# Optimization experiments

Measured on AMD Instinct MI355X. Metric: run time of the kernel, lower is better.

The kernel has to match this reference:

```python
import jax, jax.numpy as jnp
import numpy as np

N, T, D, H = 256, 128, 512, 1024


def setup_inputs() -> dict:
    key = jax.random.key(0)
    k_x, k_A, k_Wx, k_Wh, k_Wa = jax.random.split(key, 5)
    x = jax.random.normal(k_x, (N, T, D), dtype=jnp.float32)
    A = jax.random.normal(k_A, (N, H, 4, 4), dtype=jnp.float32)
    Wx = jax.random.normal(k_Wx, (D, 4 * H), dtype=jnp.float32) / np.sqrt(D)
    Wh = jax.random.normal(k_Wh, (H, 4 * H), dtype=jnp.float32) / np.sqrt(H)
    Wattn = jax.random.normal(k_Wa, (H, 4 * H), dtype=jnp.float32) / np.sqrt(H)
    b = jnp.zeros((4 * H,), dtype=jnp.float32)
    return {"x": x, "A": A, "Wx": Wx, "Wh": Wh, "Wattn": Wattn, "b": b}


def _attention_lstm(x, A, Wx, Wh, Wattn, b):
    # A: (N, H, 4, 4) -> flatten spatial to (N, H, 16)
    A_flat = A.reshape(A.shape[0], A.shape[1], -1)
    h0 = A_flat.mean(axis=2)  # (N, H)
    c0 = h0
    Hdim = h0.shape[1]
    scale = 1.0 / jnp.sqrt(jnp.asarray(Hdim, dtype=x.dtype))

    def step(carry, x_t):
        prev_h, prev_c = carry
        # scaled dot-product attention over 16 spatial locations
        scores = jnp.einsum("nh,nhs->ns", prev_h, A_flat) * scale  # (N, 16)
        w = jax.nn.softmax(scores, axis=1)
        attn = jnp.einsum("nhs,ns->nh", A_flat, w)  # (N, H)
        # fused LSTM gates
        a = x_t @ Wx + prev_h @ Wh + attn @ Wattn + b  # (N, 4H)
        i = jax.nn.sigmoid(a[:, 0:Hdim])
        f = jax.nn.sigmoid(a[:, Hdim:2 * Hdim])
        o = jax.nn.sigmoid(a[:, 2 * Hdim:3 * Hdim])
        g = jnp.tanh(a[:, 3 * Hdim:4 * Hdim])
        next_c = f * prev_c + i * g
        next_h = o * jnp.tanh(next_c)
        return (next_h, next_c), next_h

    x_tnd = jnp.swapaxes(x, 0, 1)  # (T, N, D)
    _, h_tnh = jax.lax.scan(step, (h0, c0), x_tnd)
    return jnp.swapaxes(h_tnh, 0, 1)  # (N, T, H)


def reference(x, A, Wx, Wh, Wattn, b):
    return _attention_lstm(x, A, Wx, Wh, Wattn, b)
```

## Files before the change

kernel.cpp:

```cpp
#include <hip/hip_runtime.h>
#include <math.h>

#define NB 256
#define TT 128
#define DD 512
#define HH 1024
#define KHX 1536
#define KFB 2560
#define BK 128
#define NBLK6 256
#define SCSLOT 32768
#define HSLOT (NB * HH)

typedef _Float16 half_t;
typedef _Float16 half8 __attribute__((ext_vector_type(8)));
typedef _Float16 half4v __attribute__((ext_vector_type(4)));
typedef _Float16 half2v __attribute__((ext_vector_type(2)));
typedef float f32x4 __attribute__((ext_vector_type(4)));


__global__ __launch_bounds__(256) void k_trans(const float* __restrict__ src,
        half_t* __restrict__ dst, int kstride, int koff, int nkt) {
    __shared__ half_t tile[64][65];
    int bk = blockIdx.x % nkt;
    int bn = blockIdx.x / nkt;
    int k0 = bk * 64, n0 = bn * 64;
    #pragma unroll
    for (int i = 0; i < 16; ++i) {
        int idx = i * 256 + threadIdx.x;
        int r = idx >> 6, c = idx & 63;
        tile[c][r] = (half_t)src[(size_t)(k0 + r) * 4096 + n0 + c];
    }
    __syncthreads();
    #pragma unroll
    for (int i = 0; i < 16; ++i) {
        int idx = i * 256 + threadIdx.x;
        int r = idx >> 6, c = idx & 63;
        dst[(size_t)(n0 + r) * kstride + koff + k0 + c] = tile[r][c];
    }
}

__global__ __launch_bounds__(256) void k_convX(const float* __restrict__ x,
        half_t* __restrict__ x16) {
    size_t base = ((size_t)blockIdx.x * 256 + threadIdx.x) * 32;
    #pragma unroll
    for (int u = 0; u < 4; ++u) {
        float4 a = ((const float4*)(x + base))[2 * u];
        float4 c = ((const float4*)(x + base))[2 * u + 1];
        half8 p;
        p[0] = (half_t)a.x; p[1] = (half_t)a.y; p[2] = (half_t)a.z; p[3] = (half_t)a.w;
        p[4] = (half_t)c.x; p[5] = (half_t)c.y; p[6] = (half_t)c.z; p[7] = (half_t)c.w;
        ((half8*)(x16 + base))[u] = p;
    }
}

__global__ __launch_bounds__(256) void k_convA2(const float* __restrict__ A,
        half_t* __restrict__ A16, half_t* __restrict__ AsT,
        float* __restrict__ cbuf, half_t* __restrict__ h16) {
    int n = blockIdx.x, tid = threadIdx.x;
    #pragma unroll
    for (int r = 0; r < 4; ++r) {
        int h = tid + r * 256;
        const float4* ap = (const float4*)(A + ((size_t)n * HH + h) * 16);
        float4 v0 = ap[0], v1 = ap[1], v2 = ap[2], v3 = ap[3];
        float a[16];
        a[0]=v0.x; a[1]=v0.y; a[2] =v0.z; a[3] =v0.w;
        a[4]=v1.x; a[5]=v1.y; a[6] =v1.z; a[7] =v1.w;
        a[8]=v2.x; a[9]=v2.y; a[10]=v2.z; a[11]=v2.w;
        a[12]=v3.x; a[13]=v3.y; a[14]=v3.z; a[15]=v3.w;
        float hv = 0.f;
        #pragma unroll
        for (int s = 0; s < 16; ++s) hv += a[s];
        hv *= (1.f / 16.f);
        size_t ci = (size_t)n * HH + h;
        cbuf[ci] = hv;
        h16[ci] = (half_t)hv;
        half8 q0, q1;
        #pragma unroll
        for (int s = 0; s < 8; ++s) { q0[s] = (half_t)a[s]; q1[s] = (half_t)a[s + 8]; }
        *(half8*)(A16 + ci * 16) = q0;
        *(half8*)(A16 + ci * 16 + 8) = q1;
        #pragma unroll
        for (int s = 0; s < 16; ++s)
            AsT[(size_t)n * 16 * HH + (size_t)s * HH + h] = (half_t)a[s];
    }
}

__global__ __launch_bounds__(256) void k_initsc(const half_t* __restrict__ h16,
        const half_t* __restrict__ A16,
        float* __restrict__ sc0, float* __restrict__ sc1, float* __restrict__ sc2) {
    __shared__ float sred[4][16];
    int n = blockIdx.x, tid = threadIdx.x;
    float ps[16];
    #pragma unroll
    for (int s = 0; s < 16; ++s) ps[s] = 0.f;
    #pragma unroll
    for (int r = 0; r < 4; ++r) {
        int h = tid + r * 256;
        size_t ci = (size_t)n * HH + h;
        float hv = (float)h16[ci];
        const half8* ap = (const half8*)(A16 + ci * 16);
        half8 a0 = ap[0], a1 = ap[1];
        #pragma unroll
        for (int s = 0; s < 8; ++s) {
            ps[s]     += hv * (float)a0[s];
            ps[s + 8] += hv * (float)a1[s];
        }
    }
    #pragma unroll
    for (int off = 32; off; off >>= 1)
        #pragma unroll
        for (int s = 0; s < 16; ++s) ps[s] += __shfl_xor(ps[s], off, 64);
    int wave = tid >> 6;
    if ((tid & 63) == 0)
        #pragma unroll
        for (int s = 0; s < 16; ++s) sred[wave][s] = ps[s];
    __syncthreads();
    if (tid < 16)
        sc0[(size_t)n * 16 + tid] =
            sred[0][tid] + sred[1][tid] + sred[2][tid] + sred[3][tid];
    if (tid < 112) {
        int x = 1 + tid / 16, s = tid % 16;
        sc0[((size_t)x * 256 + n) * 16 + s] = 0.f;
    }
    if (tid < 128) {
        int x = tid / 16, s = tid % 16;
        sc1[((size_t)x * 256 + n) * 16 + s] = 0.f;
        sc2[((size_t)x * 256 + n) * 16 + s] = 0.f;
    }
}

__global__ __launch_bounds__(256) void k_gemm_G(const half_t* __restrict__ AsT,
        const half_t* __restrict__ WaT, half_t* __restrict__ G16) {
    __shared__ half_t sAs[16][BK + 8];
    __shared__ half_t sB[4][16][BK + 8];
    int bid = blockIdx.x;
    int n = bid >> 6, jt = bid & 63;
    int j0 = jt * 16;
    int tid = threadIdx.x, wv = tid >> 6, lane = tid & 63;
    f32x4 acc = {};
    int srB = tid >> 2, scB = (tid & 3) * 32;
    int gB = srB >> 4, jcB = srB & 15;
    for (int it = 0; it < HH / BK; ++it) {
        int k0 = it * BK;
        if (tid < 128) {
            int r = tid >> 3, c = (tid & 7) * 16;
            const uint4* sp = (const uint4*)(AsT + (size_t)n * 16 * HH + (size_t)r * HH + k0 + c);
            uint4 u0 = sp[0], u1 = sp[1];
            *(uint4*)&sAs[r][c] = u0;
            *(uint4*)&sAs[r][c + 8] = u1;
        }
        {
            const half_t* src = WaT + ((size_t)(gB * HH + j0 + jcB)) * HH + k0 + scB;
            uint4 u0 = ((const uint4*)src)[0];
            uint4 u1 = ((const uint4*)src)[1];
            uint4 u2 = ((const uint4*)src)[2];
            uint4 u3 = ((const uint4*)src)[3];
            *((uint4*)&sB[gB][jcB][scB])      = u0;
            *((uint4*)&sB[gB][jcB][scB + 8])  = u1;
            *((uint4*)&sB[gB][jcB][scB + 16]) = u2;
            *((uint4*)&sB[gB][jcB][scB + 24]) = u3;
        }
        __syncthreads();
        int row16 = lane & 15, kg = lane >> 4;
        #pragma unroll
        for (int kc = 0; kc < BK / 32; ++kc) {
            half8 bf = *(const half8*)&sB[wv][row16][kc * 32 + kg * 8];
            half8 af = *(const half8*)&sAs[row16][kc * 32 + kg * 8];
            acc = __builtin_amdgcn_mfma_f32_16x16x32_f16(af, bf, acc, 0, 0, 0);
        }
        __syncthreads();
    }
    int col = lane & 15, rbase = (lane >> 4) * 4;
    size_t jf = (size_t)wv * HH + j0 + col;
    half4v o;
    o[0] = (half_t)acc[0]; o[1] = (half_t)acc[1];
    o[2] = (half_t)acc[2]; o[3] = (half_t)acc[3];
    *(half4v*)(G16 + ((size_t)n * 4096 + jf) * 16 + rbase) = o;
}

__global__ __launch_bounds__(256) void k_gemm_XW2(const half_t* __restrict__ x16,
        const half_t* __restrict__ WhxT, half_t* __restrict__ XW16) {
    __shared__ half_t sA[128][520];
    __shared__ half_t sB[128][72];
    int bm = blockIdx.x;
    int row0 = bm * 128;
    int tid = threadIdx.x, wv = tid >> 6, lane = tid & 63;
    int la = lane & 15, kg = lane >> 4;
    int mh = wv & 1, jh = wv >> 1;
    {
        int r = tid >> 1, hseg = tid & 1;
        const uint4* src = (const uint4*)(x16 + (size_t)(row0 + r) * DD + hseg * 256);
        #pragma unroll
        for (int i = 0; i < 16; ++i)
            *(uint4*)&sA[r][hseg * 256 + i * 8] = src[i];
    }
    __syncthreads();
    int srB = tid >> 2, scB = (tid & 3) * 16;
    for (int bj = 0; bj < 64; ++bj) {
        f32x4 acc[4][2] = {};
        for (int c = 0; c < 8; ++c) {
            {
                const uint4* sp = (const uint4*)(WhxT + (size_t)(bj * 64 + srB) * KHX + c * 64 + scB);
                *(uint4*)&sB[srB][scB] = sp[0];
            }
            __syncthreads();
            #pragma unroll
            for (int ks = 0; ks < 2; ++ks) {
                half8 b0 = *(const half8*)&sB[jh * 32 + la][ks * 32 + kg * 8];
                half8 b1 = *(const half8*)&sB[jh * 32 + 16 + la][ks * 32 + kg * 8];
                #pragma unroll
                for (int m = 0; m < 4; ++m) {
                    half8 af = *(const half8*)&sA[mh * 64 + m * 16 + la][c * 64 + ks * 32 + kg * 8];
                    acc[m][0] = __builtin_amdgcn_mfma_f32_16x16x32_f16(af, b0, acc[m][0], 0, 0, 0);
                    acc[m][1] = __builtin_amdgcn_mfma_f32_16x16x32_f16(af, b1, acc[m][1], 0, 0, 0);
                }
            }
            __syncthreads();
        }
        #pragma unroll
        for (int m = 0; m < 4; ++m)
            #pragma unroll
            for (int jt = 0; jt < 2; ++jt)
                #pragma unroll
                for (int q = 0; q < 4; ++q) {
                    int rl = mh * 64 + m * 16 + kg * 4 + q;
                    int cl = jh * 32 + jt * 16 + la;
                    sB[rl][cl] = (half_t)acc[m][jt][q];
                }
        __syncthreads();
        int col0 = bj * 64;
        int g = col0 >> 10;
        #pragma unroll
        for (int i = 0; i < 4; ++i) {
            int idx = tid + i * 256;
            int rl = idx >> 3, grp = idx & 7;
            int R = row0 + rl;
            int t = R & 127, nn = R >> 7;
            int mh2 = nn >> 7, nl2 = nn & 127;
            int jb2 = ((col0 & 1023) >> 3) + grp;
            size_t dst = ((((size_t)t * 128 + jb2) * 2 + mh2) * 128 + nl2) * 32 + g * 8;
            *(half8*)(XW16 + dst) = *(const half8*)&sB[rl][grp * 8];
        }
        __syncthreads();
    }
}


__global__ __launch_bounds__(512, 1) void k_steps6(
        const half_t* __restrict__ XW16, half_t* __restrict__ hh,
        const half_t* __restrict__ WhxT, const half_t* __restrict__ A16,
        const half_t* __restrict__ G16, const float* __restrict__ b,
        const float* __restrict__ cbuf, float* __restrict__ scr,
        float* __restrict__ out, int* __restrict__ bar) {
    __shared__ half_t W[32][1028];
    __shared__ float sm[4][128][16];
    __shared__ float pe[128][33];
    __shared__ float ps[2][128][18];

    int bid = blockIdx.x;
    int mhalf = bid & 1, jb = bid >> 1;
    int n0 = mhalf * 128;
    int tid = threadIdx.x;
    int wv = tid >> 6, lane = tid & 63;
    int la = lane & 15, kg = lane >> 4;
    int slice = bid & 7;
    int* hcnt = bar + mhalf * 32;

    {
        int wr = tid >> 4, seg = tid & 15;
        const half_t* wsrc = WhxT + (size_t)((wr >> 3) * HH + jb * 8 + (wr & 7)) * KHX
                           + DD + seg * 64;
        #pragma unroll
        for (int i = 0; i < 8; ++i)
            *(uint4*)&W[wr][seg * 64 + i * 8] = ((const uint4*)wsrc)[i];
    }

    int n_l = tid & 127, jg2 = tid >> 7;
    int n = n0 + n_l;
    int jbase = jb * 8 + jg2 * 2;
    half8 gq[4][4];
    #pragma unroll
    for (int g = 0; g < 4; ++g) {
        const half8* gsrc = (const half8*)(G16 + ((size_t)n * 4096 + g * HH + jbase) * 16);
        #pragma unroll
        for (int i = 0; i < 4; ++i) gq[g][i] = gsrc[i];
    }
    half8 aq[4];
    {
        const half8* asrc = (const half8*)(A16 + ((size_t)n * HH + jbase) * 16);
        #pragma unroll
        for (int i = 0; i < 4; ++i) aq[i] = asrc[i];
    }
    float bb[4][2];
    #pragma unroll
    for (int g = 0; g < 4; ++g) {
        bb[g][0] = b[g * HH + jbase];
        bb[g][1] = b[g * HH + jbase + 1];
    }
    float creg[2];
    creg[0] = cbuf[(size_t)n * HH + jbase];
    creg[1] = cbuf[(size_t)n * HH + jbase + 1];

    __threadfence();
    __syncthreads();

    for (int t = 0; t < TT; ++t) {
        const half_t* hcur = hh + (size_t)t * HSLOT;
        unsigned* hnext = (unsigned*)(hh + (size_t)(t + 1) * HSLOT);
        const float* scc = scr + (size_t)t * SCSLOT;
        float* scn = scr + (size_t)(t + 1) * SCSLOT;

        half2v xwv[4];
        {
            const half_t* xwp = XW16 + ((((size_t)t * 128 + jb) * 2 + mhalf) * 128 + n_l) * 32;
            #pragma unroll
            for (int g = 0; g < 4; ++g) xwv[g] = *(const half2v*)(xwp + g * 8 + jg2 * 2);
        }

        if (t > 0) {
            int tgt = 4 * t;
            int guard = 0;
            for (;;) {
                int v = (lane < 32)
                    ? __hip_atomic_load(&hcnt[lane], __ATOMIC_RELAXED, __HIP_MEMORY_SCOPE_AGENT)
                    : tgt;
                if (__all(v >= tgt)) break;
                __builtin_amdgcn_s_sleep(2);
                if (++guard > (1 << 18)) break;
            }
        }
        __builtin_amdgcn_sched_barrier(0);

        {
            const float* p0 = scc + ((size_t)(jg2 * 2) * 256 + n) * 16;
            const float* p1 = scc + ((size_t)(jg2 * 2 + 1) * 256 + n) * 16;
            #pragma unroll
            for (int i = 0; i < 4; ++i) {
                float4 a = ((const float4*)p0)[i];
                float4 c = ((const float4*)p1)[i];
                float4 o;
                o.x = a.x + c.x; o.y = a.y + c.y; o.z = a.z + c.z; o.w = a.w + c.w;
                *(float4*)&sm[jg2][n_l][4 * i] = o;
            }
        }
        __syncthreads();
        float w16[16];
        {
            float sc[16];
            #pragma unroll
            for (int i = 0; i < 4; ++i) {
                float4 q0 = *(const float4*)&sm[0][n_l][4 * i];
                float4 q1 = *(const float4*)&sm[1][n_l][4 * i];
                float4 q2 = *(const float4*)&sm[2][n_l][4 * i];
                float4 q3 = *(const float4*)&sm[3][n_l][4 * i];
                sc[4 * i + 0] = q0.x + q1.x + q2.x + q3.x;
                sc[4 * i + 1] = q0.y + q1.y + q2.y + q3.y;
                sc[4 * i + 2] = q0.z + q1.z + q2.z + q3.z;
                sc[4 * i + 3] = q0.w + q1.w + q2.w + q3.w;
            }
            float m = -1e30f;
            #pragma unroll
            for (int s = 0; s < 16; ++s) { sc[s] *= 0.03125f; m = fmaxf(m, sc[s]); }
            float den = 0.f;
            #pragma unroll
            for (int s = 0; s < 16; ++s) { sc[s] = expf(sc[s] - m); den += sc[s]; }
            float inv = 1.f / den;
            #pragma unroll
            for (int s = 0; s < 16; ++s) w16[s] = sc[s] * inv;
        }

        f32x4 acc0 = {}, acc1 = {};
        {
            const half_t* hrow = hcur + (size_t)(n0 + wv * 16 + la) * HH + kg * 8;
            #pragma unroll
            for (int c = 0; c < 32; ++c) {
                half8 af = *(const half8*)(hrow + c * 32);
                half8 b0 = *(const half8*)&W[la][c * 32 + kg * 8];
                half8 b1 = *(const half8*)&W[16 + la][c * 32 + kg * 8];
                acc0 = __builtin_amdgcn_mfma_f32_16x16x32_f16(af, b0, acc0, 0, 0, 0);
                acc1 = __builtin_amdgcn_mfma_f32_16x16x32_f16(af, b1, acc1, 0, 0, 0);
            }
        }

        __syncthreads();
        #pragma unroll
        for (int q = 0; q < 4; ++q) {
            pe[wv * 16 + kg * 4 + q][la]      = acc0[q];
            pe[wv * 16 + kg * 4 + q][16 + la] = acc1[q];
        }
        __syncthreads();

        float v[4][2];
        #pragma unroll
        for (int g = 0; g < 4; ++g) {
            #pragma unroll
            for (int jj = 0; jj < 2; ++jj) {
                float a0 = 0.f;
                #pragma unroll
                for (int s = 0; s < 16; ++s)
                    a0 += w16[s] * (float)gq[g][jj * 2 + (s >> 3)][s & 7];
                v[g][jj] = pe[n_l][g * 8 + jg2 * 2 + jj] + bb[g][jj]
                         + (float)xwv[g][jj] + a0;
            }
        }
        float hv[2];
        #pragma unroll
        for (int jj = 0; jj < 2; ++jj) {
            float ig = 1.f / (1.f + expf(-v[0][jj]));
            float fg = 1.f / (1.f + expf(-v[1][jj]));
            float og = 1.f / (1.f + expf(-v[2][jj]));
            float gg = tanhf(v[3][jj]);
            float cn = fg * creg[jj] + ig * gg;
            creg[jj] = cn;
            hv[jj] = og * tanhf(cn);
        }
        {
            float2 o2; o2.x = hv[0]; o2.y = hv[1];
            *(float2*)(out + ((size_t)n * TT + t) * HH + jbase) = o2;
            union { half2v h2; unsigned u; } cv;
            cv.h2[0] = (half_t)hv[0]; cv.h2[1] = (half_t)hv[1];
            __hip_atomic_store(hnext + (((size_t)n * HH + jbase) >> 1), cv.u,
                               __ATOMIC_RELAXED, __HIP_MEMORY_SCOPE_AGENT);
        }
        float p[16];
        #pragma unroll
        for (int s = 0; s < 16; ++s)
            p[s] = hv[0] * (float)aq[s >> 3][s & 7]
                 + hv[1] * (float)aq[2 + (s >> 3)][s & 7];
        int pair = jg2 >> 1;
        if ((jg2 & 1) == 0) {
            #pragma unroll
            for (int s = 0; s < 16; ++s) ps[pair][n_l][s] = p[s];
        }
        __syncthreads();
        if ((jg2 & 1) == 1) {
            #pragma unroll
            for (int s = 0; s < 16; ++s) ps[pair][n_l][s] += p[s];
        }
        __syncthreads();
        #pragma unroll
        for (int i = 0; i < 4; ++i) {
            int slot = tid * 4 + i;
            int nn = slot >> 4, s = slot & 15;
            atomicAdd(scn + ((size_t)slice * 256 + n0 + nn) * 16 + s,
                      ps[0][nn][s] + ps[1][nn][s]);
        }

        __syncthreads();
        if (tid == 0)
            __hip_atomic_fetch_add(&hcnt[jb >> 2], 1, __ATOMIC_RELAXED,
                                   __HIP_MEMORY_SCOPE_AGENT);
    }
}


__global__ __launch_bounds__(256) void k_convA(const float* __restrict__ A,
        half_t* __restrict__ A16, half_t* __restrict__ AsT,
        float* __restrict__ cbuf, half_t* __restrict__ h16,
        float* __restrict__ sc0, float* __restrict__ sc1, float* __restrict__ sc2) {
    __shared__ float sred[4][16];
    int n = blockIdx.x, tid = threadIdx.x;
    float ps[16];
    #pragma unroll
    for (int s = 0; s < 16; ++s) ps[s] = 0.f;
    #pragma unroll
    for (int r = 0; r < 4; ++r) {
        int h = tid + r * 256;
        const float4* ap = (const float4*)(A + ((size_t)n * HH + h) * 16);
        float4 v0 = ap[0], v1 = ap[1], v2 = ap[2], v3 = ap[3];
        float a[16];
        a[0]=v0.x; a[1]=v0.y; a[2] =v0.z; a[3] =v0.w;
        a[4]=v1.x; a[5]=v1.y; a[6] =v1.z; a[7] =v1.w;
        a[8]=v2.x; a[9]=v2.y; a[10]=v2.z; a[11]=v2.w;
        a[12]=v3.x; a[13]=v3.y; a[14]=v3.z; a[15]=v3.w;
        float hv = 0.f;
        #pragma unroll
        for (int s = 0; s < 16; ++s) hv += a[s];
        hv *= (1.f / 16.f);
        size_t ci = (size_t)n * HH + h;
        cbuf[ci] = hv;
        h16[ci] = (half_t)hv;
        half8 q0, q1;
        #pragma unroll
        for (int s = 0; s < 8; ++s) { q0[s] = (half_t)a[s]; q1[s] = (half_t)a[s + 8]; }
        *(half8*)(A16 + ci * 16) = q0;
        *(half8*)(A16 + ci * 16 + 8) = q1;
        #pragma unroll
        for (int s = 0; s < 16; ++s)
            AsT[(size_t)n * 16 * HH + (size_t)s * HH + h] = (half_t)a[s];
        #pragma unroll
        for (int s = 0; s < 16; ++s) ps[s] += hv * a[s];
    }
    #pragma unroll
    for (int off = 32; off; off >>= 1)
        #pragma unroll
        for (int s = 0; s < 16; ++s) ps[s] += __shfl_xor(ps[s], off, 64);
    int wave = tid >> 6;
    if ((tid & 63) == 0)
        #pragma unroll
        for (int s = 0; s < 16; ++s) sred[wave][s] = ps[s];
    __syncthreads();
    if (tid < 16) {
        sc0[n * 16 + tid] = sred[0][tid] + sred[1][tid] + sred[2][tid] + sred[3][tid];
        sc1[n * 16 + tid] = 0.f;
        sc2[n * 16 + tid] = 0.f;
    }
}

union LdsS {
    struct {
        half_t sA[32][BK + 8];
        half_t sB[4][16][BK + 8];
    } s;
    float pe[4][32][16];
};

__global__ __launch_bounds__(256) void k_step(const float* __restrict__ x,
        const half_t* __restrict__ h16c, half_t* __restrict__ h16n,
        const half_t* __restrict__ WhxT, const half_t* __restrict__ A16,
        const half_t* __restrict__ G16, const float* __restrict__ b,
        float* __restrict__ cbuf, const float* __restrict__ scC,
        float* __restrict__ scN, float* __restrict__ scZ,
        float* __restrict__ out, int t) {
    __shared__ LdsS L;
    __shared__ float wlds[32][16];
    int bid = blockIdx.x;
    int xcd = bid & 7, slot = bid >> 3;
    int mtile = slot & 7, jtile = slot >> 3;
    int n0 = mtile * 32;
    int j0 = xcd * 128 + jtile * 16;
    int tid = threadIdx.x, wv = tid >> 6, lane = tid & 63;

    if (bid < 16) scZ[bid * 256 + tid] = 0.f;
    if (tid < 32) {
        int n = n0 + tid;
        const float4* sp = (const float4*)(scC + n * 16);
        float4 u0 = sp[0], u1 = sp[1], u2 = sp[2], u3 = sp[3];
        float sc[16] = {u0.x, u0.y, u0.z, u0.w, u1.x, u1.y, u1.z, u1.w,
                        u2.x, u2.y, u2.z, u2.w, u3.x, u3.y, u3.z, u3.w};
        float m = -1e30f;
        #pragma unroll
        for (int s = 0; s < 16; ++s) { sc[s] *= 0.03125f; m = fmaxf(m, sc[s]); }
        float den = 0.f;
        #pragma unroll
        for (int s = 0; s < 16; ++s) { sc[s] = expf(sc[s] - m); den += sc[s]; }
        float inv = 1.f / den;
        #pragma unroll
        for (int s = 0; s < 16; ++s) wlds[tid][s] = sc[s] * inv;
    }

    f32x4 acc[2] = {};
    int srA = tid >> 3, scA = (tid & 7) * 16;
    int srB = tid >> 2, scB = (tid & 3) * 32;
    int gB = srB >> 4, jcB = srB & 15;

    for (int it = 0; it < KHX / BK; ++it) {
        int k0 = it * BK;
        {
            int n = n0 + srA;
            if (k0 < DD) {
                const float* src = x + ((size_t)n * TT + t) * DD + k0 + scA;
                float4 v0 = ((const float4*)src)[0];
                float4 v1 = ((const float4*)src)[1];
                float4 v2 = ((const float4*)src)[2];
                float4 v3 = ((const float4*)src)[3];
                half8 p0, p1;
                p0[0] = (half_t)v0.x; p0[1] = (half_t)v0.y; p0[2] = (half_t)v0.z; p0[3] = (half_t)v0.w;
                p0[4] = (half_t)v1.x; p0[5] = (half_t)v1.y; p0[6] = (half_t)v1.z; p0[7] = (half_t)v1.w;
                p1[0] = (half_t)v2.x; p1[1] = (half_t)v2.y; p1[2] = (half_t)v2.z; p1[3] = (half_t)v2.w;
                p1[4] = (half_t)v3.x; p1[5] = (half_t)v3.y; p1[6] = (half_t)v3.z; p1[7] = (half_t)v3.w;
                *(half8*)&L.s.sA[srA][scA]     = p0;
                *(half8*)&L.s.sA[srA][scA + 8] = p1;
            } else {
                const half_t* srch = h16c + (size_t)n * HH + (k0 - DD) + scA;
                uint4 u0 = ((const uint4*)srch)[0];
                uint4 u1 = ((const uint4*)srch)[1];
                *((uint4*)&L.s.sA[srA][scA])     = u0;
                *((uint4*)&L.s.sA[srA][scA + 8]) = u1;
            }
        }
        {
            const half_t* src = WhxT + ((size_t)(gB * HH + j0 + jcB)) * KHX + k0 + scB;
            uint4 u0 = ((const uint4*)src)[0];
            uint4 u1 = ((const uint4*)src)[1];
            uint4 u2 = ((const uint4*)src)[2];
            uint4 u3 = ((const uint4*)src)[3];
            *((uint4*)&L.s.sB[gB][jcB][scB])      = u0;
            *((uint4*)&L.s.sB[gB][jcB][scB + 8])  = u1;
            *((uint4*)&L.s.sB[gB][jcB][scB + 16]) = u2;
            *((uint4*)&L.s.sB[gB][jcB][scB + 24]) = u3;
        }
        __syncthreads();
        int row16 = lane & 15, kg = lane >> 4;
        #pragma unroll
        for (int kc = 0; kc < BK / 32; ++kc) {
            half8 bf = *(const half8*)&L.s.sB[wv][row16][kc * 32 + kg * 8];
            #pragma unroll
            for (int m = 0; m < 2; ++m) {
                half8 af = *(const half8*)&L.s.sA[row16 + m * 16][kc * 32 + kg * 8];
                acc[m] = __builtin_amdgcn_mfma_f32_16x16x32_f16(af, bf, acc[m], 0, 0, 0);
            }
        }
        __syncthreads();
    }
    {
        int col = lane & 15, rbase = (lane >> 4) * 4;
        #pragma unroll
        for (int m = 0; m < 2; ++m)
            #pragma unroll
            for (int q = 0; q < 4; ++q)
                L.pe[wv][m * 16 + rbase + q][col] = acc[m][q];
    }
    __syncthreads();
    #pragma unroll
    for (int q2 = 0; q2 < 2; ++q2) {
        int idx = tid + q2 * 256;
        int r = idx >> 4, jc = idx & 15;
        int n = n0 + r, j = j0 + jc;
        float wv16[16];
        #pragma unroll
        for (int s = 0; s < 16; ++s) wv16[s] = wlds[r][s];
        float v[4];
        v[0] = L.pe[0][r][jc] + b[j];
        v[1] = L.pe[1][r][jc] + b[HH + j];
        v[2] = L.pe[2][r][jc] + b[2 * HH + j];
        v[3] = L.pe[3][r][jc] + b[3 * HH + j];
        #pragma unroll
        for (int g = 0; g < 4; ++g) {
            const half8* gq = (const half8*)(G16 + ((size_t)n * 4096 + g * HH + j) * 16);
            half8 ga = gq[0], gb2 = gq[1];
            float a0 = 0.f;
            #pragma unroll
            for (int s = 0; s < 8; ++s)
                a0 += wv16[s] * (float)ga[s] + wv16[s + 8] * (float)gb2[s];
            v[g] += a0;
        }
        float ig = 1.f / (1.f + expf(-v[0]));
        float fg = 1.f / (1.f + expf(-v[1]));
        float og = 1.f / (1.f + expf(-v[2]));
        float gg = tanhf(v[3]);
        size_t ci = (size_t)n * HH + j;
        float cp = cbuf[ci];
        float cn = fg * cp + ig * gg;
        cbuf[ci] = cn;
        float hv = og * tanhf(cn);
        out[((size_t)n * TT + t) * HH + j] = hv;
        h16n[ci] = (half_t)hv;
        const half8* ap = (const half8*)(A16 + ci * 16);
        half8 a0 = ap[0], a1 = ap[1];
        float p[16];
        #pragma unroll
        for (int s = 0; s < 8; ++s) { p[s] = hv * (float)a0[s]; p[s + 8] = hv * (float)a1[s]; }
        #pragma unroll
        for (int msk = 1; msk < 16; msk <<= 1)
            #pragma unroll
            for (int s = 0; s < 16; ++s) p[s] += __shfl_xor(p[s], msk, 64);
        float myp = 0.f;
        #pragma unroll
        for (int s = 0; s < 16; ++s) myp = (jc == s) ? p[s] : myp;
        atomicAdd(scN + n * 16 + jc, myp);
    }
}


__global__ __launch_bounds__(256) void fb_wconv(const float* __restrict__ Wx,
        const float* __restrict__ Wh, const float* __restrict__ Wa,
        half_t* __restrict__ WT) {
    __shared__ half_t tile[64][65];
    int bk = blockIdx.x % 40;
    int bn = blockIdx.x / 40;
    int k0 = bk * 64, n0 = bn * 64;
    #pragma unroll
    for (int i = 0; i < 16; ++i) {
        int idx = i * 256 + threadIdx.x;
        int r = idx >> 6, c = idx & 63;
        int k = k0 + r, n = n0 + c;
        float v;
        if (k < DD)            v = Wx[(size_t)k * 4096 + n];
        else if (k < DD + HH)  v = Wh[(size_t)(k - DD) * 4096 + n];
        else                   v = Wa[(size_t)(k - DD - HH) * 4096 + n];
        tile[c][r] = (half_t)v;
    }
    __syncthreads();
    #pragma unroll
    for (int i = 0; i < 16; ++i) {
        int idx = i * 256 + threadIdx.x;
        int r = idx >> 6, c = idx & 63;
        WT[(size_t)(n0 + r) * KFB + k0 + c] = tile[r][c];
    }
}

__global__ __launch_bounds__(256) void fb_init(const float* __restrict__ A,
        float* __restrict__ h0, float* __restrict__ c0) {
    int n = blockIdx.x;
    #pragma unroll
    for (int r = 0; r < 4; ++r) {
        int h = threadIdx.x + r * 256;
        const float4* ap = (const float4*)(A + ((size_t)n * HH + h) * 16);
        float s = 0.f;
        #pragma unroll
        for (int q = 0; q < 4; ++q) {
            float4 v = ap[q];
            s += v.x + v.y + v.z + v.w;
        }
        s *= (1.f / 16.f);
        h0[n * HH + h] = s;
        c0[n * HH + h] = s;
    }
}

__global__ __launch_bounds__(256) void fb_attn(const float* __restrict__ A,
        const float* __restrict__ hprev, long long hstride,
        half_t* __restrict__ h16, half_t* __restrict__ attn16) {
    __shared__ float sh[HH];
    __shared__ float sred[4][16];
    int n = blockIdx.x;
    const float* hp = hprev + (size_t)n * hstride;
    #pragma unroll
    for (int r = 0; r < 4; ++r) {
        int h = threadIdx.x + r * 256;
        float v = hp[h];
        sh[h] = v;
        h16[n * HH + h] = (half_t)v;
    }
    __syncthreads();
    float a[4][16];
    float ps[16];
    #pragma unroll
    for (int s = 0; s < 16; ++s) ps[s] = 0.f;
    #pragma unroll
    for (int r = 0; r < 4; ++r) {
        int h = threadIdx.x + r * 256;
        const float4* ap = (const float4*)(A + ((size_t)n * HH + h) * 16);
        float4 v0 = ap[0], v1 = ap[1], v2 = ap[2], v3 = ap[3];
        a[r][0] = v0.x;  a[r][1] = v0.y;  a[r][2]  = v0.z;  a[r][3]  = v0.w;
        a[r][4] = v1.x;  a[r][5] = v1.y;  a[r][6]  = v1.z;  a[r][7]  = v1.w;
        a[r][8] = v2.x;  a[r][9] = v2.y;  a[r][10] = v2.z;  a[r][11] = v2.w;
        a[r][12] = v3.x; a[r][13] = v3.y; a[r][14] = v3.z;  a[r][15] = v3.w;
        float hh = sh[h];
        #pragma unroll
        for (int s = 0; s < 16; ++s) ps[s] += hh * a[r][s];
    }
    #pragma unroll
    for (int off = 32; off; off >>= 1)
        #pragma unroll
        for (int s = 0; s < 16; ++s) ps[s] += __shfl_xor(ps[s], off, 64);
    int wave = threadIdx.x >> 6;
    if ((threadIdx.x & 63) == 0)
        #pragma unroll
        for (int s = 0; s < 16; ++s) sred[wave][s] = ps[s];
    __syncthreads();
    float sc[16], m = -1e30f;
    #pragma unroll
    for (int s = 0; s < 16; ++s) {
        sc[s] = (sred[0][s] + sred[1][s] + sred[2][s] + sred[3][s]) * 0.03125f;
        m = fmaxf(m, sc[s]);
    }
    float den = 0.f;
    #pragma unroll
    for (int s = 0; s < 16; ++s) { sc[s] = expf(sc[s] - m); den += sc[s]; }
    float inv = 1.f / den;
    #pragma unroll
    for (int r = 0; r < 4; ++r) {
        int h = threadIdx.x + r * 256;
        float acc = 0.f;
        #pragma unroll
        for (int s = 0; s < 16; ++s) acc += a[r][s] * sc[s];
        attn16[n * HH + h] = (half_t)(acc * inv);
    }
}

union LdsFB {
    struct {
        half_t sA[32][BK + 8];
        half_t sB[4][16][BK + 8];
    } s;
    float pe[4][32][16];
};

__global__ __launch_bounds__(256) void fb_gemm(const float* __restrict__ x,
        const half_t* __restrict__ h16, const half_t* __restrict__ attn16,
        const half_t* __restrict__ WT, const float* __restrict__ b,
        float* __restrict__ cbuf, float* __restrict__ out, int t) {
    __shared__ LdsFB L;
    int bid = blockIdx.x;
    int xcd = bid & 7;
    int slot = bid >> 3;
    int mtile = slot & 7;
    int jtile = slot >> 3;
    int m0 = mtile * 32;
    int j0 = xcd * 128 + jtile * 16;
    int tid = threadIdx.x;
    int wv = tid >> 6, lane = tid & 63;
    f32x4 acc[2] = {};
    int srA = tid >> 3, scA = (tid & 7) * 16;
    int srB = tid >> 2, scB = (tid & 3) * 32;
    int gB = srB >> 4, jcB = srB & 15;
    for (int it = 0; it < KFB / BK; ++it) {
        int k0 = it * BK;
        {
            int n = m0 + srA;
            if (k0 < DD) {
                const float* src = x + ((size_t)n * TT + t) * DD + k0 + scA;
                float4 v0 = ((const float4*)src)[0];
                float4 v1 = ((const float4*)src)[1];
                float4 v2 = ((const float4*)src)[2];
                float4 v3 = ((const float4*)src)[3];
                half8 p0, p1;
                p0[0] = (half_t)v0.x; p0[1] = (half_t)v0.y; p0[2] = (half_t)v0.z; p0[3] = (half_t)v0.w;
                p0[4] = (half_t)v1.x; p0[5] = (half_t)v1.y; p0[6] = (half_t)v1.z; p0[7] = (half_t)v1.w;
                p1[0] = (half_t)v2.x; p1[1] = (half_t)v2.y; p1[2] = (half_t)v2.z; p1[3] = (half_t)v2.w;
                p1[4] = (half_t)v3.x; p1[5] = (half_t)v3.y; p1[6] = (half_t)v3.z; p1[7] = (half_t)v3.w;
                *(half8*)&L.s.sA[srA][scA]     = p0;
                *(half8*)&L.s.sA[srA][scA + 8] = p1;
            } else {
                const half_t* srch = (k0 < DD + HH)
                    ? (h16    + (size_t)n * HH + (k0 - DD)      + scA)
                    : (attn16 + (size_t)n * HH + (k0 - DD - HH) + scA);
                uint4 u0 = ((const uint4*)srch)[0];
                uint4 u1 = ((const uint4*)srch)[1];
                *((uint4*)&L.s.sA[srA][scA])     = u0;
                *((uint4*)&L.s.sA[srA][scA + 8]) = u1;
            }
        }
        {
            const half_t* src = WT + ((size_t)(gB * HH + j0 + jcB)) * KFB + k0 + scB;
            uint4 u0 = ((const uint4*)src)[0];
            uint4 u1 = ((const uint4*)src)[1];
            uint4 u2 = ((const uint4*)src)[2];
            uint4 u3 = ((const uint4*)src)[3];
            *((uint4*)&L.s.sB[gB][jcB][scB])      = u0;
            *((uint4*)&L.s.sB[gB][jcB][scB + 8])  = u1;
            *((uint4*)&L.s.sB[gB][jcB][scB + 16]) = u2;
            *((uint4*)&L.s.sB[gB][jcB][scB + 24]) = u3;
        }
        __syncthreads();
        int row16 = lane & 15, kg = lane >> 4;
        #pragma unroll
        for (int kc = 0; kc < BK / 32; ++kc) {
            half8 bf = *(const half8*)&L.s.sB[wv][row16][kc * 32 + kg * 8];
            #pragma unroll
            for (int m = 0; m < 2; ++m) {
                half8 af = *(const half8*)&L.s.sA[row16 + m * 16][kc * 32 + kg * 8];
                acc[m] = __builtin_amdgcn_mfma_f32_16x16x32_f16(af, bf, acc[m], 0, 0, 0);
            }
        }
        __syncthreads();
    }
    {
        int col = lane & 15, rbase = (lane >> 4) * 4;
        #pragma unroll
        for (int m = 0; m < 2; ++m)
            #pragma unroll
            for (int q = 0; q < 4; ++q)
                L.pe[wv][m * 16 + rbase + q][col] = acc[m][q];
    }
    __syncthreads();
    #pragma unroll
    for (int q2 = 0; q2 < 2; ++q2) {
        int idx = tid + q2 * 256;
        int r = idx >> 4, jc = idx & 15;
        int n = m0 + r, j = j0 + jc;
        float vi = L.pe[0][r][jc] + b[j];
        float vf = L.pe[1][r][jc] + b[HH + j];
        float vo = L.pe[2][r][jc] + b[2 * HH + j];
        float vg = L.pe[3][r][jc] + b[3 * HH + j];
        float ig = 1.f / (1.f + expf(-vi));
        float fg = 1.f / (1.f + expf(-vf));
        float og = 1.f / (1.f + expf(-vo));
        float gg = tanhf(vg);
        size_t ci = (size_t)n * HH + j;
        float cp = cbuf[ci];
        float cn = fg * cp + ig * gg;
        cbuf[ci] = cn;
        out[((size_t)n * TT + t) * HH + j] = og * tanhf(cn);
    }
}


extern "C" void kernel_launch(void* const* d_in, const int* in_sizes, int n_in,
                              void* d_out, int out_size, void* d_ws, size_t ws_size,
                              hipStream_t stream) {
    const float* x  = (const float*)d_in[0];
    const float* A  = (const float*)d_in[1];
    const float* Wx = (const float*)d_in[2];
    const float* Wh = (const float*)d_in[3];
    const float* Wa = (const float*)d_in[4];
    const float* b  = (const float*)d_in[5];
    float* out = (float*)d_out;
    char* ws = (char*)d_ws;

    int maxb = 0;
    hipError_t oe = hipOccupancyMaxActiveBlocksPerMultiprocessor(&maxb, k_steps6, 512, 0);
    bool persistent_ok = (oe == hipSuccess && maxb >= 1);

    if (ws_size >= 460112128ULL && persistent_ok) {
        half_t* WhxT = (half_t*)(ws);
        half_t* WaT  = (half_t*)(ws + 12582912);
        half_t* A16  = (half_t*)(ws + 20971520);
        half_t* AsT  = (half_t*)(ws + 29360128);
        half_t* G16  = (half_t*)(ws + 37748736);
        float*  cb   = (float*) (ws + 72351744);
        half_t* x16  = (half_t*)(ws + 73449472);
        int*    bar  = (int*)   (ws + 107003904);
        half_t* XW16 = (half_t*)(ws + 107004160);
        half_t* HHr  = (half_t*)(ws + 375439616);
        float*  SCr  = (float*) (ws + 443072768);

        half_t* hh0 = HHr;

        hipLaunchKernelGGL(k_trans, dim3(8 * 64),  dim3(256), 0, stream, Wx, WhxT, KHX, 0,   8);
        hipLaunchKernelGGL(k_trans, dim3(16 * 64), dim3(256), 0, stream, Wh, WhxT, KHX, 512, 16);
        hipLaunchKernelGGL(k_trans, dim3(16 * 64), dim3(256), 0, stream, Wa, WaT,  HH,  0,   16);
        hipLaunchKernelGGL(k_convX, dim3(2048), dim3(256), 0, stream, x, x16);
        hipLaunchKernelGGL(k_convA2, dim3(256), dim3(256), 0, stream, A, A16, AsT, cb, hh0);
        hipLaunchKernelGGL(k_gemm_G, dim3(NB * 64), dim3(256), 0, stream, AsT, WaT, G16);
        hipLaunchKernelGGL(k_gemm_XW2, dim3(256), dim3(256), 0, stream, x16, WhxT, XW16);
        hipMemsetAsync(bar, 0, 256, stream);
        hipMemsetAsync(SCr, 0, 17039360, stream);
        hipLaunchKernelGGL(k_initsc, dim3(256), dim3(256), 0, stream, hh0, A16,
                           SCr, SCr + SCSLOT, SCr + 2 * SCSLOT);
        hipLaunchKernelGGL(k_steps6, dim3(NBLK6), dim3(512), 0, stream,
                           XW16, HHr, WhxT, A16, G16, b, cb, SCr, out, bar);
    } else if (ws_size >= 73449472ULL) {
        half_t* WhxT = (half_t*)(ws);
        half_t* WaT  = (half_t*)(ws + 12582912);
        half_t* A16  = (half_t*)(ws + 20971520);
        half_t* AsT  = (half_t*)(ws + 29360128);
        half_t* G16  = (half_t*)(ws + 37748736);
        half_t* h16a = (half_t*)(ws + 71303168);
        half_t* h16b = (half_t*)(ws + 71827456);
        float*  cb   = (float*) (ws + 72351744);
        float*  sc0  = (float*) (ws + 73400320);
        float*  sc1  = (float*) (ws + 73416704);
        float*  sc2  = (float*) (ws + 73433088);
        float* scb[3] = {sc0, sc1, sc2};

        hipLaunchKernelGGL(k_trans, dim3(8 * 64),  dim3(256), 0, stream, Wx, WhxT, KHX, 0,   8);
        hipLaunchKernelGGL(k_trans, dim3(16 * 64), dim3(256), 0, stream, Wh, WhxT, KHX, 512, 16);
        hipLaunchKernelGGL(k_trans, dim3(16 * 64), dim3(256), 0, stream, Wa, WaT,  HH,  0,   16);
        hipLaunchKernelGGL(k_convA, dim3(256), dim3(256), 0, stream,
                           A, A16, AsT, cb, h16a, sc0, sc1, sc2);
        hipLaunchKernelGGL(k_gemm_G, dim3(NB * 64), dim3(256), 0, stream, AsT, WaT, G16);
        for (int t = 0; t < TT; ++t) {
            float* scC = scb[t % 3];
            float* scN = scb[(t + 1) % 3];
            float* scZ = scb[(t + 2) % 3];
            half_t* h16c = (t & 1) ? h16b : h16a;
            half_t* h16n = (t & 1) ? h16a : h16b;
            hipLaunchKernelGGL(k_step, dim3(512), dim3(256), 0, stream,
                               x, h16c, h16n, WhxT, A16, G16, b, cb, scC, scN, scZ, out, t);
        }
    } else {
        half_t* WT  = (half_t*)ws;
        float*  h0  = (float*)(ws + 20971520);
        float*  cb  = (float*)(ws + 22020096);
        half_t* h16 = (half_t*)(ws + 23068672);
        half_t* a16 = (half_t*)(ws + 23592960);
        hipLaunchKernelGGL(fb_wconv, dim3(2560), dim3(256), 0, stream, Wx, Wh, Wa, WT);
        hipLaunchKernelGGL(fb_init, dim3(256), dim3(256), 0, stream, A, h0, cb);
        for (int t = 0; t < TT; ++t) {
            const float* hp = (t == 0) ? h0 : (out + (size_t)(t - 1) * HH);
            long long hstride = (t == 0) ? (long long)HH : (long long)TT * HH;
            hipLaunchKernelGGL(fb_attn, dim3(256), dim3(256), 0, stream, A, hp, hstride, h16, a16);
            hipLaunchKernelGGL(fb_gemm, dim3(512), dim3(256), 0, stream,
                               x, h16, a16, WT, b, cb, out, t);
        }
    }
}
```

Before: 4.635 ms.

## Compute attention scores per home row with counter sync instead of atomics

The persistent step kernel no longer builds next-step attention scores by atomically accumulating partial dot products from every block into sliced buffers. Instead, each block computes the full score vector for one batch row from the current hidden state and publishes it, and other blocks wait on a per-half counter before reading. This removes the init-score kernel, the large memset and the per-step atomicAdd traffic, at the cost of an extra spin-wait per step. The XW GEMM is also reverted to a 2D grid of small tiles, and nontemporal loads and stores are used for the XW input and the output.

```diff
diff --git a/kernel.cpp b/kernel.cpp
--- a/kernel.cpp
+++ b/kernel.cpp
@@ -8,9 +8,9 @@
 #define KHX 1536
 #define KFB 2560
 #define BK 128
-#define NBLK6 256
-#define SCSLOT 32768
+#define NBLK7 256
 #define HSLOT (NB * HH)
+#define SCSLOT2 (NB * 16)
 
 typedef _Float16 half_t;
 typedef _Float16 half8 __attribute__((ext_vector_type(8)));
@@ -83,50 +83,6 @@
         #pragma unroll
         for (int s = 0; s < 16; ++s)
             AsT[(size_t)n * 16 * HH + (size_t)s * HH + h] = (half_t)a[s];
-    }
-}
-
-__global__ __launch_bounds__(256) void k_initsc(const half_t* __restrict__ h16,
-        const half_t* __restrict__ A16,
-        float* __restrict__ sc0, float* __restrict__ sc1, float* __restrict__ sc2) {
-    __shared__ float sred[4][16];
-    int n = blockIdx.x, tid = threadIdx.x;
-    float ps[16];
-    #pragma unroll
-    for (int s = 0; s < 16; ++s) ps[s] = 0.f;
-    #pragma unroll
-    for (int r = 0; r < 4; ++r) {
-        int h = tid + r * 256;
-        size_t ci = (size_t)n * HH + h;
-        float hv = (float)h16[ci];
-        const half8* ap = (const half8*)(A16 + ci * 16);
-        half8 a0 = ap[0], a1 = ap[1];
-        #pragma unroll
-        for (int s = 0; s < 8; ++s) {
-            ps[s]     += hv * (float)a0[s];
-            ps[s + 8] += hv * (float)a1[s];
-        }
-    }
-    #pragma unroll
-    for (int off = 32; off; off >>= 1)
-        #pragma unroll
-        for (int s = 0; s < 16; ++s) ps[s] += __shfl_xor(ps[s], off, 64);
-    int wave = tid >> 6;
-    if ((tid & 63) == 0)
-        #pragma unroll
-        for (int s = 0; s < 16; ++s) sred[wave][s] = ps[s];
-    __syncthreads();
-    if (tid < 16)
-        sc0[(size_t)n * 16 + tid] =
-            sred[0][tid] + sred[1][tid] + sred[2][tid] + sred[3][tid];
-    if (tid < 112) {
-        int x = 1 + tid / 16, s = tid % 16;
-        sc0[((size_t)x * 256 + n) * 16 + s] = 0.f;
-    }
-    if (tid < 128) {
-        int x = tid / 16, s = tid % 16;
-        sc1[((size_t)x * 256 + n) * 16 + s] = 0.f;
-        sc2[((size_t)x * 256 + n) * 16 + s] = 0.f;
     }
 }
 
@@ -179,93 +135,92 @@
     *(half4v*)(G16 + ((size_t)n * 4096 + jf) * 16 + rbase) = o;
 }
 
-__global__ __launch_bounds__(256) void k_gemm_XW2(const half_t* __restrict__ x16,
+__global__ __launch_bounds__(256) void k_gemm_XW(const half_t* __restrict__ x16,
         const half_t* __restrict__ WhxT, half_t* __restrict__ XW16) {
-    __shared__ half_t sA[128][520];
-    __shared__ half_t sB[128][72];
-    int bm = blockIdx.x;
+    __shared__ half_t sA[128][72];
+    __shared__ half_t sB[64][72];
+    int bid = blockIdx.x;
+    int bm = bid & 255;
+    int bj = bid >> 8;
     int row0 = bm * 128;
+    int col0 = bj * 64;
     int tid = threadIdx.x, wv = tid >> 6, lane = tid & 63;
     int la = lane & 15, kg = lane >> 4;
     int mh = wv & 1, jh = wv >> 1;
-    {
-        int r = tid >> 1, hseg = tid & 1;
-        const uint4* src = (const uint4*)(x16 + (size_t)(row0 + r) * DD + hseg * 256);
-        #pragma unroll
-        for (int i = 0; i < 16; ++i)
-            *(uint4*)&sA[r][hseg * 256 + i * 8] = src[i];
+    f32x4 acc[4][2] = {};
+    int srA = tid >> 1, scA = (tid & 1) * 32;
+    int srB = tid >> 2, scB = (tid & 3) * 16;
+    for (int c = 0; c < 8; ++c) {
+        {
+            const uint4* sp = (const uint4*)(x16 + (size_t)(row0 + srA) * DD + c * 64 + scA);
+            uint4 u0 = sp[0], u1 = sp[1];
+            *(uint4*)&sA[srA][scA] = u0;
+            *(uint4*)&sA[srA][scA + 8] = u1;
+        }
+        {
+            const uint4* sp = (const uint4*)(WhxT + (size_t)(col0 + srB) * KHX + c * 64 + scB);
+            *(uint4*)&sB[srB][scB] = sp[0];
+        }
+        __syncthreads();
+        #pragma unroll
+        for (int ks = 0; ks < 2; ++ks) {
+            half8 b0 = *(const half8*)&sB[jh * 32 + la][ks * 32 + kg * 8];
+            half8 b1 = *(const half8*)&sB[jh * 32 + 16 + la][ks * 32 + kg * 8];
+            #pragma unroll
+            for (int m = 0; m < 4; ++m) {
+                half8 af = *(const half8*)&sA[mh * 64 + m * 16 + la][ks * 32 + kg * 8];
+                acc[m][0] = __builtin_amdgcn_mfma_f32_16x16x32_f16(af, b0, acc[m][0], 0, 0, 0);
+                acc[m][1] = __builtin_amdgcn_mfma_f32_16x16x32_f16(af, b1, acc[m][1], 0, 0, 0);
+            }
+        }
+        __syncthreads();
     }
     __syncthreads();
-    int srB = tid >> 2, scB = (tid & 3) * 16;
-    for (int bj = 0; bj < 64; ++bj) {
-        f32x4 acc[4][2] = {};
-        for (int c = 0; c < 8; ++c) {
-            {
-                const uint4* sp = (const uint4*)(WhxT + (size_t)(bj * 64 + srB) * KHX + c * 64 + scB);
-                *(uint4*)&sB[srB][scB] = sp[0];
-            }
-            __syncthreads();
-            #pragma unroll
-            for (int ks = 0; ks < 2; ++ks) {
-                half8 b0 = *(const half8*)&sB[jh * 32 + la][ks * 32 + kg * 8];
-                half8 b1 = *(const half8*)&sB[jh * 32 + 16 + la][ks * 32 + kg * 8];
-                #pragma unroll
-                for (int m = 0; m < 4; ++m) {
-                    half8 af = *(const half8*)&sA[mh * 64 + m * 16 + la][c * 64 + ks * 32 + kg * 8];
-                    acc[m][0] = __builtin_amdgcn_mfma_f32_16x16x32_f16(af, b0, acc[m][0], 0, 0, 0);
-                    acc[m][1] = __builtin_amdgcn_mfma_f32_16x16x32_f16(af, b1, acc[m][1], 0, 0, 0);
-                }
-            }
-            __syncthreads();
-        }
-        #pragma unroll
-        for (int m = 0; m < 4; ++m)
-            #pragma unroll
-            for (int jt = 0; jt < 2; ++jt)
-                #pragma unroll
-                for (int q = 0; q < 4; ++q) {
-                    int rl = mh * 64 + m * 16 + kg * 4 + q;
-                    int cl = jh * 32 + jt * 16 + la;
-                    sB[rl][cl] = (half_t)acc[m][jt][q];
-                }
-        __syncthreads();
-        int col0 = bj * 64;
-        int g = col0 >> 10;
-        #pragma unroll
-        for (int i = 0; i < 4; ++i) {
-            int idx = tid + i * 256;
-            int rl = idx >> 3, grp = idx & 7;
-            int R = row0 + rl;
-            int t = R & 127, nn = R >> 7;
-            int mh2 = nn >> 7, nl2 = nn & 127;
-            int jb2 = ((col0 & 1023) >> 3) + grp;
-            size_t dst = ((((size_t)t * 128 + jb2) * 2 + mh2) * 128 + nl2) * 32 + g * 8;
-            *(half8*)(XW16 + dst) = *(const half8*)&sB[rl][grp * 8];
-        }
-        __syncthreads();
-    }
-}
-
-
-__global__ __launch_bounds__(512, 1) void k_steps6(
+    half_t (*Cl)[72] = sA;
+    #pragma unroll
+    for (int m = 0; m < 4; ++m)
+        #pragma unroll
+        for (int jt = 0; jt < 2; ++jt)
+            #pragma unroll
+            for (int q = 0; q < 4; ++q) {
+                int rl = mh * 64 + m * 16 + kg * 4 + q;
+                int cl = jh * 32 + jt * 16 + la;
+                Cl[rl][cl] = (half_t)acc[m][jt][q];
+            }
+    __syncthreads();
+    int g = col0 >> 10;
+    #pragma unroll
+    for (int i = 0; i < 4; ++i) {
+        int idx = tid + i * 256;
+        int rl = idx >> 3, grp = idx & 7;
+        int R = row0 + rl;
+        int t = R & 127, nn = R >> 7;
+        int mh2 = nn >> 7, nl2 = nn & 127;
+        int jb2 = ((col0 & 1023) >> 3) + grp;
+        size_t dst = ((((size_t)t * 128 + jb2) * 2 + mh2) * 128 + nl2) * 32 + g * 8;
+        *(half8*)(XW16 + dst) = *(const half8*)&Cl[rl][grp * 8];
+    }
+}
+
+
+__global__ __launch_bounds__(512, 1) void k_steps7(
         const half_t* __restrict__ XW16, half_t* __restrict__ hh,
         const half_t* __restrict__ WhxT, const half_t* __restrict__ A16,
         const half_t* __restrict__ G16, const float* __restrict__ b,
         const float* __restrict__ cbuf, float* __restrict__ scr,
         float* __restrict__ out, int* __restrict__ bar) {
     __shared__ half_t W[32][1028];
-    __shared__ float sm[4][128][16];
+    __shared__ float red[8][16];
     __shared__ float pe[128][33];
-    __shared__ float ps[2][128][18];
 
     int bid = blockIdx.x;
     int mhalf = bid & 1, jb = bid >> 1;
     int n0 = mhalf * 128;
     int tid = threadIdx.x;
-    int wv = tid >> 6, lane = tid & 63;
+    int wvi = tid >> 6, lane = tid & 63;
     int la = lane & 15, kg = lane >> 4;
-    int slice = bid & 7;
     int* hcnt = bar + mhalf * 32;
+    int* scnt = bar + 64 + mhalf * 32;
 
     {
         int wr = tid >> 4, seg = tid & 15;
@@ -278,6 +233,7 @@
 
     int n_l = tid & 127, jg2 = tid >> 7;
     int n = n0 + n_l;
+    int n_home = n0 + jb;
     int jbase = jb * 8 + jg2 * 2;
     half8 gq[4][4];
     #pragma unroll
@@ -285,12 +241,6 @@
         const half8* gsrc = (const half8*)(G16 + ((size_t)n * 4096 + g * HH + jbase) * 16);
         #pragma unroll
         for (int i = 0; i < 4; ++i) gq[g][i] = gsrc[i];
-    }
-    half8 aq[4];
-    {
-        const half8* asrc = (const half8*)(A16 + ((size_t)n * HH + jbase) * 16);
-        #pragma unroll
-        for (int i = 0; i < 4; ++i) aq[i] = asrc[i];
     }
     float bb[4][2];
     #pragma unroll
@@ -308,14 +258,17 @@
     for (int t = 0; t < TT; ++t) {
         const half_t* hcur = hh + (size_t)t * HSLOT;
         unsigned* hnext = (unsigned*)(hh + (size_t)(t + 1) * HSLOT);
-        const float* scc = scr + (size_t)t * SCSLOT;
-        float* scn = scr + (size_t)(t + 1) * SCSLOT;
+        float* scw = scr + (size_t)t * SCSLOT2;
 
         half2v xwv[4];
         {
             const half_t* xwp = XW16 + ((((size_t)t * 128 + jb) * 2 + mhalf) * 128 + n_l) * 32;
             #pragma unroll
-            for (int g = 0; g < 4; ++g) xwv[g] = *(const half2v*)(xwp + g * 8 + jg2 * 2);
+            for (int g = 0; g < 4; ++g) {
+                unsigned u = __builtin_nontemporal_load((const unsigned*)(xwp + g * 8 + jg2 * 2));
+                union { unsigned uu; half2v h2; } cv; cv.uu = u;
+                xwv[g] = cv.h2;
+            }
         }
 
         if (t > 0) {
@@ -333,46 +286,41 @@
         __builtin_amdgcn_sched_barrier(0);
 
         {
-            const float* p0 = scc + ((size_t)(jg2 * 2) * 256 + n) * 16;
-            const float* p1 = scc + ((size_t)(jg2 * 2 + 1) * 256 + n) * 16;
-            #pragma unroll
-            for (int i = 0; i < 4; ++i) {
-                float4 a = ((const float4*)p0)[i];
-                float4 c = ((const float4*)p1)[i];
-                float4 o;
-                o.x = a.x + c.x; o.y = a.y + c.y; o.z = a.z + c.z; o.w = a.w + c.w;
-                *(float4*)&sm[jg2][n_l][4 * i] = o;
-            }
-        }
-        __syncthreads();
-        float w16[16];
-        {
-            float sc[16];
-            #pragma unroll
-            for (int i = 0; i < 4; ++i) {
-                float4 q0 = *(const float4*)&sm[0][n_l][4 * i];
-                float4 q1 = *(const float4*)&sm[1][n_l][4 * i];
-                float4 q2 = *(const float4*)&sm[2][n_l][4 * i];
-                float4 q3 = *(const float4*)&sm[3][n_l][4 * i];
-                sc[4 * i + 0] = q0.x + q1.x + q2.x + q3.x;
-                sc[4 * i + 1] = q0.y + q1.y + q2.y + q3.y;
-                sc[4 * i + 2] = q0.z + q1.z + q2.z + q3.z;
-                sc[4 * i + 3] = q0.w + q1.w + q2.w + q3.w;
-            }
-            float m = -1e30f;
-            #pragma unroll
-            for (int s = 0; s < 16; ++s) { sc[s] *= 0.03125f; m = fmaxf(m, sc[s]); }
-            float den = 0.f;
-            #pragma unroll
-            for (int s = 0; s < 16; ++s) { sc[s] = expf(sc[s] - m); den += sc[s]; }
-            float inv = 1.f / den;
-            #pragma unroll
-            for (int s = 0; s < 16; ++s) w16[s] = sc[s] * inv;
-        }
+            half2v h2 = *(const half2v*)(hcur + (size_t)n_home * HH + 2 * tid);
+            float h0 = (float)h2[0], h1 = (float)h2[1];
+            const half8* ap = (const half8*)(A16 + ((size_t)n_home * HH + 2 * tid) * 16);
+            half8 a0 = ap[0], a1 = ap[1], a2 = ap[2], a3 = ap[3];
+            float p[16];
+            #pragma unroll
+            for (int s = 0; s < 8; ++s) {
+                p[s]     = h0 * (float)a0[s] + h1 * (float)a2[s];
+                p[s + 8] = h0 * (float)a1[s] + h1 * (float)a3[s];
+            }
+            #pragma unroll
+            for (int off = 32; off; off >>= 1)
+                #pragma unroll
+                for (int s = 0; s < 16; ++s) p[s] += __shfl_xor(p[s], off, 64);
+            if (lane == 0) {
+                #pragma unroll
+                for (int s = 0; s < 16; ++s) red[wvi][s] = p[s];
+            }
+        }
+        __syncthreads();
+        if (tid < 16) {
+            float s8 = 0.f;
+            #pragma unroll
+            for (int w = 0; w < 8; ++w) s8 += red[w][tid];
+            __hip_atomic_store(&scw[n_home * 16 + tid], s8,
+                               __ATOMIC_RELAXED, __HIP_MEMORY_SCOPE_AGENT);
+        }
+        __syncthreads();
+        if (tid == 0)
+            __hip_atomic_fetch_add(&scnt[jb >> 2], 1, __ATOMIC_RELAXED,
+                                   __HIP_MEMORY_SCOPE_AGENT);
 
         f32x4 acc0 = {}, acc1 = {};
         {
-            const half_t* hrow = hcur + (size_t)(n0 + wv * 16 + la) * HH + kg * 8;
+            const half_t* hrow = hcur + (size_t)(n0 + wvi * 16 + la) * HH + kg * 8;
             #pragma unroll
             for (int c = 0; c < 32; ++c) {
                 half8 af = *(const half8*)(hrow + c * 32);
@@ -382,14 +330,44 @@
                 acc1 = __builtin_amdgcn_mfma_f32_16x16x32_f16(af, b1, acc1, 0, 0, 0);
             }
         }
-
         __syncthreads();
         #pragma unroll
         for (int q = 0; q < 4; ++q) {
-            pe[wv * 16 + kg * 4 + q][la]      = acc0[q];
-            pe[wv * 16 + kg * 4 + q][16 + la] = acc1[q];
-        }
-        __syncthreads();
+            pe[wvi * 16 + kg * 4 + q][la]      = acc0[q];
+            pe[wvi * 16 + kg * 4 + q][16 + la] = acc1[q];
+        }
+        __syncthreads();
+
+        {
+            int tgt = 4 * (t + 1);
+            int guard = 0;
+            for (;;) {
+                int v = (lane < 32)
+                    ? __hip_atomic_load(&scnt[lane], __ATOMIC_RELAXED, __HIP_MEMORY_SCOPE_AGENT)
+                    : tgt;
+                if (__all(v >= tgt)) break;
+                __builtin_amdgcn_s_sleep(2);
+                if (++guard > (1 << 18)) break;
+            }
+        }
+        __builtin_amdgcn_sched_barrier(0);
+
+        float w16[16];
+        {
+            const float4* sp = (const float4*)(scr + (size_t)t * SCSLOT2 + (size_t)n * 16);
+            float4 q0 = sp[0], q1 = sp[1], q2 = sp[2], q3 = sp[3];
+            float sc[16] = {q0.x, q0.y, q0.z, q0.w, q1.x, q1.y, q1.z, q1.w,
+                            q2.x, q2.y, q2.z, q2.w, q3.x, q3.y, q3.z, q3.w};
+            float m = -1e30f;
+            #pragma unroll
+            for (int s = 0; s < 16; ++s) { sc[s] *= 0.03125f; m = fmaxf(m, sc[s]); }
+            float den = 0.f;
+            #pragma unroll
+            for (int s = 0; s < 16; ++s) { sc[s] = expf(sc[s] - m); den += sc[s]; }
+            float inv = 1.f / den;
+            #pragma unroll
+            for (int s = 0; s < 16; ++s) w16[s] = sc[s] * inv;
+        }
 
         float v[4][2];
         #pragma unroll
@@ -416,35 +394,14 @@
             hv[jj] = og * tanhf(cn);
         }
         {
-            float2 o2; o2.x = hv[0]; o2.y = hv[1];
-            *(float2*)(out + ((size_t)n * TT + t) * HH + jbase) = o2;
+            union { float2 f2; unsigned long long u; } ov;
+            ov.f2.x = hv[0]; ov.f2.y = hv[1];
+            __builtin_nontemporal_store(ov.u,
+                (unsigned long long*)(out + ((size_t)n * TT + t) * HH + jbase));
             union { half2v h2; unsigned u; } cv;
             cv.h2[0] = (half_t)hv[0]; cv.h2[1] = (half_t)hv[1];
             __hip_atomic_store(hnext + (((size_t)n * HH + jbase) >> 1), cv.u,
                                __ATOMIC_RELAXED, __HIP_MEMORY_SCOPE_AGENT);
-        }
-        float p[16];
-        #pragma unroll
-        for (int s = 0; s < 16; ++s)
-            p[s] = hv[0] * (float)aq[s >> 3][s & 7]
-                 + hv[1] * (float)aq[2 + (s >> 3)][s & 7];
-        int pair = jg2 >> 1;
-        if ((jg2 & 1) == 0) {
-            #pragma unroll
-            for (int s = 0; s < 16; ++s) ps[pair][n_l][s] = p[s];
-        }
-        __syncthreads();
-        if ((jg2 & 1) == 1) {
-            #pragma unroll
-            for (int s = 0; s < 16; ++s) ps[pair][n_l][s] += p[s];
-        }
-        __syncthreads();
-        #pragma unroll
-        for (int i = 0; i < 4; ++i) {
-            int slot = tid * 4 + i;
-            int nn = slot >> 4, s = slot & 15;
-            atomicAdd(scn + ((size_t)slice * 256 + n0 + nn) * 16 + s,
-                      ps[0][nn][s] + ps[1][nn][s]);
         }
 
         __syncthreads();
@@ -892,7 +849,7 @@
     char* ws = (char*)d_ws;
 
     int maxb = 0;
-    hipError_t oe = hipOccupancyMaxActiveBlocksPerMultiprocessor(&maxb, k_steps6, 512, 0);
+    hipError_t oe = hipOccupancyMaxActiveBlocksPerMultiprocessor(&maxb, k_steps7, 512, 0);
     bool persistent_ok = (oe == hipSuccess && maxb >= 1);
 
     if (ws_size >= 460112128ULL && persistent_ok) {
@@ -902,8 +859,8 @@
         half_t* AsT  = (half_t*)(ws + 29360128);
         half_t* G16  = (half_t*)(ws + 37748736);
         float*  cb   = (float*) (ws + 72351744);
+        int*    bar  = (int*)   (ws + 73400320);
         half_t* x16  = (half_t*)(ws + 73449472);
-        int*    bar  = (int*)   (ws + 107003904);
         half_t* XW16 = (half_t*)(ws + 107004160);
         half_t* HHr  = (half_t*)(ws + 375439616);
         float*  SCr  = (float*) (ws + 443072768);
@@ -916,12 +873,9 @@
         hipLaunchKernelGGL(k_convX, dim3(2048), dim3(256), 0, stream, x, x16);
         hipLaunchKernelGGL(k_convA2, dim3(256), dim3(256), 0, stream, A, A16, AsT, cb, hh0);
         hipLaunchKernelGGL(k_gemm_G, dim3(NB * 64), dim3(256), 0, stream, AsT, WaT, G16);
-        hipLaunchKernelGGL(k_gemm_XW2, dim3(256), dim3(256), 0, stream, x16, WhxT, XW16);
-        hipMemsetAsync(bar, 0, 256, stream);
-        hipMemsetAsync(SCr, 0, 17039360, stream);
-        hipLaunchKernelGGL(k_initsc, dim3(256), dim3(256), 0, stream, hh0, A16,
-                           SCr, SCr + SCSLOT, SCr + 2 * SCSLOT);
-        hipLaunchKernelGGL(k_steps6, dim3(NBLK6), dim3(512), 0, stream,
+        hipLaunchKernelGGL(k_gemm_XW, dim3(256 * 64), dim3(256), 0, stream, x16, WhxT, XW16);
+        hipMemsetAsync(bar, 0, 1024, stream);
+        hipLaunchKernelGGL(k_steps7, dim3(NBLK7), dim3(512), 0, stream,
                            XW16, HHr, WhxT, A16, G16, b, cb, SCr, out, bar);
     } else if (ws_size >= 73449472ULL) {
         half_t* WhxT = (half_t*)(ws);
```

Result: no change. 4.639 ms (+0.1%).
